# Performance work log

Hardware: AMD Instinct MI355X
Metric: run time of the kernel (lower is better)

The kernel has to match this reference:

```python
import jax, jax.numpy as jnp
import numpy as np

B, S, E = 4, 1024, 1024
H = 16
HD = E // H  # 64
NEXP = 8
FF = 4 * E
EPS = 1e-5


def _ln(x, g, b):
    m = jnp.mean(x, axis=-1, keepdims=True)
    v = jnp.var(x, axis=-1, keepdims=True)
    return (x - m) * jax.lax.rsqrt(v + EPS) * g + b


def setup_inputs() -> dict:
    key = jax.random.key(0)
    ks = jax.random.split(key, 16)
    sd = 0.02
    inp = {
        "x": jax.random.normal(ks[0], (B, S, E), jnp.float32),
        # per-head Q/K/V linears, stacked over heads: [H, E, HD]
        "wq": jax.random.normal(ks[1], (H, E, HD), jnp.float32) * sd,
        "bq": jnp.zeros((H, HD), jnp.float32),
        "wk": jax.random.normal(ks[2], (H, E, HD), jnp.float32) * sd,
        "bk": jnp.zeros((H, HD), jnp.float32),
        "wv": jax.random.normal(ks[3], (H, E, HD), jnp.float32) * sd,
        "bv": jnp.zeros((H, HD), jnp.float32),
        "wp": jax.random.normal(ks[4], (E, E), jnp.float32) * sd,
        "bp": jnp.zeros((E,), jnp.float32),
        "ln1_g": jnp.ones((E,), jnp.float32),
        "ln1_b": jnp.zeros((E,), jnp.float32),
        "ln2_g": jnp.ones((E,), jnp.float32),
        "ln2_b": jnp.zeros((E,), jnp.float32),
        "wr": jax.random.normal(ks[5], (E, NEXP), jnp.float32) * sd,
        "br": jnp.zeros((NEXP,), jnp.float32),
        # experts stacked: [NEXP, E, FF], [NEXP, FF, E]
        "w1": jax.random.normal(ks[6], (NEXP, E, FF), jnp.float32) * sd,
        "b1": jnp.zeros((NEXP, FF), jnp.float32),
        "w2": jax.random.normal(ks[7], (NEXP, FF, E), jnp.float32) * sd,
        "b2": jnp.zeros((NEXP, E), jnp.float32),
    }
    return inp


def _block(x, wq, bq, wk, bk, wv, bv, wp, bp, ln1_g, ln1_b, ln2_g, ln2_b,
           wr, br, w1, b1, w2, b2):
    # --- multi-head causal attention (per-head Q/K/V, concat, project) ---
    q = jnp.einsum('bse,hed->bhsd', x, wq) + bq[None, :, None, :]
    k = jnp.einsum('bse,hed->bhsd', x, wk) + bk[None, :, None, :]
    v = jnp.einsum('bse,hed->bhsd', x, wv) + bv[None, :, None, :]
    scores = jnp.einsum('bhsd,bhtd->bhst', q, k) / jnp.sqrt(jnp.float32(HD))
    causal = jnp.tril(jnp.ones((S, S), bool))
    scores = jnp.where(causal[None, None], scores, -jnp.inf)
    attn = jax.nn.softmax(scores, axis=-1)
    heads = jnp.einsum('bhst,bhtd->bhsd', attn, v)
    # concat heads (dim order matches torch.cat over head list)
    cat = heads.transpose(0, 2, 1, 3).reshape(B, S, E)
    attn_out = cat @ wp + bp
    # --- residual + LN1 ---
    h = _ln(attn_out + x, ln1_g, ln1_b)
    # --- MoE: router probs weight ALL experts densely (indices unused) ---
    probs = jax.nn.softmax(h @ wr + br, axis=-1)  # [B,S,NEXP]
    mid = jax.nn.relu(jnp.einsum('bse,nef->bnsf', h, w1) + b1[None, :, None, :])
    eo = jnp.einsum('bnsf,nfe->bnse', mid, w2) + b2[None, :, None, :]
    moe_out = jnp.einsum('bnse,bsn->bse', eo, probs)
    # --- residual uses ORIGINAL inputs (as in source) + LN2 ---
    return _ln(moe_out + x, ln2_g, ln2_b)


def reference(x, wq, bq, wk, bk, wv, bv, wp, bp, ln1_g, ln1_b, ln2_g, ln2_b,
              wr, br, w1, b1, w2, b2):
    return _block(x, wq, bq, wk, bk, wv, bv, wp, bp, ln1_g, ln1_b,
                  ln2_g, ln2_b, wr, br, w1, b1, w2, b2)
```

## Files before the change

kernel.cpp:

```cpp
#include <hip/hip_runtime.h>
#include <hip/hip_bf16.h>

typedef unsigned short u16;
typedef unsigned int u32;
typedef __attribute__((ext_vector_type(8))) short bf16x8;
typedef __attribute__((ext_vector_type(4))) float f32x4;

#define DEV static __device__ __forceinline__

DEV u16 f2b(float f) {
  union { float f; u32 u; } v; v.f = f;
  return (u16)((v.u + 0x7fffu + ((v.u >> 16) & 1u)) >> 16);
}

DEV void gload16(const void* g, void* l) {
  __builtin_amdgcn_global_load_lds(
      (const __attribute__((address_space(1))) u32*)g,
      (__attribute__((address_space(3))) u32*)l, 16, 0, 0);
}

__global__ __launch_bounds__(256) void cvt_bf16(const float* __restrict__ s,
                                                u16* __restrict__ d) {
  const long i = ((long)blockIdx.x * 256 + threadIdx.x) * 4;
  const float4 v = *(const float4*)&s[i];
  ushort4 o;
  o.x = f2b(v.x); o.y = f2b(v.y); o.z = f2b(v.z); o.w = f2b(v.w);
  *(ushort4*)&d[i] = o;
}

__global__ __launch_bounds__(256) void tpose_bf16(const float* __restrict__ src,
                                                  u16* __restrict__ dst, int R,
                                                  int C, long sStride,
                                                  long dStride, long ldd) {
  __shared__ float tl[32][33];
  const float* s = src + (long)blockIdx.z * sStride;
  u16* d = dst + (long)blockIdx.z * dStride;
  const int c0 = blockIdx.x * 32, r0 = blockIdx.y * 32;
  const int tx = threadIdx.x, ty = threadIdx.y;
  const int tid = ty * 32 + tx;
#pragma unroll
  for (int k = 0; k < 4; k++)
    tl[ty + k * 8][tx] = s[(long)(r0 + ty + k * 8) * C + c0 + tx];
  __syncthreads();
  const int oc = tid >> 3, orb = (tid & 7) * 4;
  ushort4 o;
  o.x = f2b(tl[orb + 0][oc]);
  o.y = f2b(tl[orb + 1][oc]);
  o.z = f2b(tl[orb + 2][oc]);
  o.w = f2b(tl[orb + 3][oc]);
  *(ushort4*)&d[(long)(c0 + oc) * ldd + r0 + orb] = o;
}

enum { EQKV, EPROJ, EFF1, EFF2, EFF2I };

template <int EPI>
__global__ __launch_bounds__(256, 3) void gemm_bt(
    const u16* __restrict__ A, const u16* __restrict__ Bt, int K, long lda,
    long ldb, const float* __restrict__ c0, const float* __restrict__ c1,
    const float* __restrict__ c2, const float* __restrict__ aux,
    float* __restrict__ fout, u16* __restrict__ o0, u16* __restrict__ o1,
    u16* __restrict__ o2, int ebase, long ldc) {
  __shared__ u16 As[12288], Bs[12288];
  long zc = 0;
  if constexpr (EPI == EFF2 || EPI == EFF2I) {
    const long z = blockIdx.z;
    A += z * (long)K;
    Bt += z * (long)K;
    fout += z * 4194304;
  }
  if constexpr (EPI == EFF1) {
    Bt += (long)blockIdx.z * 4194304;
    zc = (long)blockIdx.z * 4096;
  }
  const int tid = threadIdx.x;
  const int m0 = blockIdx.y * 128, n0 = blockIdx.x * 128;
  const int w = tid >> 6, l = tid & 63;
  const int wm = (w >> 1) * 64, wn = (w & 1) * 64;
  const int lr = l & 15, lh = l >> 4;
  f32x4 acc[4][4] = {};
  const u16* AgB = A + (long)(m0 + (tid >> 2)) * lda + (tid & 3) * 8;
  const u16* BgB = Bt + (long)(n0 + (tid >> 2)) * ldb + (tid & 3) * 8;
  const long rsA = 64 * lda, rsB = 64 * ldb;
  u16* asd = As + tid * 8;
  u16* bsd = Bs + tid * 8;
  const int nt = K >> 5;
  gload16(AgB, asd);             gload16(AgB + rsA, asd + 2048);
  gload16(BgB, bsd);             gload16(BgB + rsB, bsd + 2048);
  gload16(AgB + 32, asd + 4096); gload16(AgB + rsA + 32, asd + 6144);
  gload16(BgB + 32, bsd + 4096); gload16(BgB + rsB + 32, bsd + 6144);
  asm volatile("s_waitcnt vmcnt(4)" ::: "memory");
  __builtin_amdgcn_sched_barrier(0);
  __builtin_amdgcn_s_barrier();
  __builtin_amdgcn_sched_barrier(0);
  int oc = 0, on = 4096, ot = 8192;
  for (int t = 0; t < nt; ++t) {
    const int ks = (t + 2 < nt ? t + 2 : nt - 1) * 32;
    gload16(AgB + ks, asd + ot);
    gload16(AgB + rsA + ks, asd + ot + 2048);
    gload16(BgB + ks, bsd + ot);
    gload16(BgB + rsB + ks, bsd + ot + 2048);
    bf16x8 af[4], bfr[4];
#pragma unroll
    for (int i = 0; i < 4; i++)
      af[i] = *(const bf16x8*)&As[oc + (wm + i * 16 + lr) * 32 + lh * 8];
#pragma unroll
    for (int j = 0; j < 4; j++)
      bfr[j] = *(const bf16x8*)&Bs[oc + (wn + j * 16 + lr) * 32 + lh * 8];
    __builtin_amdgcn_s_setprio(1);
#pragma unroll
    for (int i = 0; i < 4; i++)
#pragma unroll
      for (int j = 0; j < 4; j++)
        acc[i][j] = __builtin_amdgcn_mfma_f32_16x16x32_bf16(af[i], bfr[j],
                                                            acc[i][j], 0, 0, 0);
    __builtin_amdgcn_s_setprio(0);
    asm volatile("s_waitcnt vmcnt(4)" ::: "memory");
    __builtin_amdgcn_sched_barrier(0);
    __builtin_amdgcn_s_barrier();
    __builtin_amdgcn_sched_barrier(0);
    const int tmp = oc; oc = on; on = ot; ot = tmp;
  }
  asm volatile("s_waitcnt vmcnt(0)" ::: "memory");
#pragma unroll
  for (int j = 0; j < 4; j++) {
    const int col = n0 + wn + j * 16 + lr;
#pragma unroll
    for (int i = 0; i < 4; i++)
#pragma unroll
      for (int r = 0; r < 4; r++) {
        const int row = m0 + wm + i * 16 + lh * 4 + r;
        float v = acc[i][j][r];
        if constexpr (EPI == EQKV) {
          const int which = col >> 10, hd = col & 1023;
          const float vb =
              v + ((which == 0) ? c0 : (which == 1) ? c1 : c2)[hd];
          const int b = row >> 10, s = row & 1023;
          const int h = hd >> 6, d = hd & 63;
          const long bh = b * 16 + h;
          if (which == 0)
            o0[(bh * 1024 + s) * 64 + d] = f2b(vb * 0.125f);
          else if (which == 1)
            o1[(bh * 1024 + s) * 64 + d] = f2b(vb);
          else
            o2[bh * 65536 + (long)d * 1024 + s] = f2b(vb);
        } else if constexpr (EPI == EPROJ) {
          const long idx = (long)row * 1024 + col;
          fout[idx] = v + c0[col] + aux[idx];
        } else if constexpr (EPI == EFF1) {
          const int e = ebase + blockIdx.z;
          const float t = v + c0[(long)e * 4096 + col];
          const float rl = t > 0.f ? t : 0.f;
          const float pw = aux[(long)row * 8 + e];
          o0[(long)row * ldc + zc + col] = f2b(rl * pw);
        } else {
          const long idx = (long)row * 1024 + col;
          if constexpr (EPI == EFF2I)
            fout[idx] = v;
          else
            fout[idx] = fout[idx] + v;
        }
      }
  }
}

__global__ __launch_bounds__(256) void attn_fwd(const u16* __restrict__ Qb,
                                                const u16* __restrict__ Kb,
                                                const u16* __restrict__ Vt,
                                                u16* __restrict__ Cat) {
  const int tid = threadIdx.x;
  const int w = tid >> 6, l = tid & 63;
  const int lr = l & 15, lh = l >> 4;
  const int bh = blockIdx.y;
  const int q0 = blockIdx.x * 64 + w * 16;
  const u16* Qp = Qb + (long)bh * 65536;
  const u16* Kp = Kb + (long)bh * 65536;
  const u16* Vp = Vt + (long)bh * 65536;
  const bf16x8 qf0 = *(const bf16x8*)&Qp[(q0 + lr) * 64 + lh * 8];
  const bf16x8 qf1 = *(const bf16x8*)&Qp[(q0 + lr) * 64 + 32 + lh * 8];
  const int q = q0 + lr;
  f32x4 o[4] = {};
  float m = -1e30f, ssum = 0.f;
  const int hi = lh >> 1;
  const int s0 = ((lh & 1) * 2) * 16 + lr;
  const int s1 = ((lh & 1) * 2 + 1) * 16 + lr;
  const int nkt = q0 / 32 + 1;
  for (int kt = 0; kt < nkt; kt++) {
    const int t0 = kt * 32;
    f32x4 sc[2];
#pragma unroll
    for (int ts = 0; ts < 2; ts++) {
      const bf16x8 kf0 = *(const bf16x8*)&Kp[(t0 + ts * 16 + lr) * 64 + lh * 8];
      const bf16x8 kf1 =
          *(const bf16x8*)&Kp[(t0 + ts * 16 + lr) * 64 + 32 + lh * 8];
      f32x4 c = {};
      c = __builtin_amdgcn_mfma_f32_16x16x32_bf16(kf0, qf0, c, 0, 0, 0);
      c = __builtin_amdgcn_mfma_f32_16x16x32_bf16(kf1, qf1, c, 0, 0, 0);
      sc[ts] = c;
    }
#pragma unroll
    for (int ts = 0; ts < 2; ts++)
#pragma unroll
      for (int r = 0; r < 4; r++)
        if (t0 + ts * 16 + lh * 4 + r > q) sc[ts][r] = -1e30f;
    float mt = fmaxf(fmaxf(fmaxf(sc[0][0], sc[0][1]), fmaxf(sc[0][2], sc[0][3])),
                     fmaxf(fmaxf(sc[1][0], sc[1][1]), fmaxf(sc[1][2], sc[1][3])));
    mt = fmaxf(mt, __shfl_xor(mt, 16));
    mt = fmaxf(mt, __shfl_xor(mt, 32));
    const float mnew = fmaxf(m, mt);
    const float scl = __expf(m - mnew);
    m = mnew;
    float p0[4], p1[4], ps = 0.f;
#pragma unroll
    for (int r = 0; r < 4; r++) {
      p0[r] = __expf(sc[0][r] - mnew);
      p1[r] = __expf(sc[1][r] - mnew);
      ps += p0[r] + p1[r];
    }
    ssum = ssum * scl + ps;
    u16 pb[8];
#pragma unroll
    for (int r = 0; r < 4; r++) {
      const float a0 = __shfl(p0[r], s0), b0 = __shfl(p1[r], s0);
      const float a1 = __shfl(p0[r], s1), b1 = __shfl(p1[r], s1);
      pb[r] = f2b(hi ? b0 : a0);
      pb[r + 4] = f2b(hi ? b1 : a1);
    }
#pragma unroll
    for (int dt = 0; dt < 4; dt++)
#pragma unroll
      for (int r = 0; r < 4; r++) o[dt][r] *= scl;
    const bf16x8 pf = *(const bf16x8*)pb;
    __builtin_amdgcn_s_setprio(1);
#pragma unroll
    for (int dt = 0; dt < 4; dt++) {
      const bf16x8 vf =
          *(const bf16x8*)&Vp[(dt * 16 + lr) * 1024 + t0 + lh * 8];
      o[dt] = __builtin_amdgcn_mfma_f32_16x16x32_bf16(vf, pf, o[dt], 0, 0, 0);
    }
    __builtin_amdgcn_s_setprio(0);
  }
  ssum += __shfl_xor(ssum, 16);
  ssum += __shfl_xor(ssum, 32);
  const float inv = 1.f / ssum;
  const int b = bh >> 4, h = bh & 15;
#pragma unroll
  for (int dt = 0; dt < 4; dt++) {
    ushort4 st;
    st.x = f2b(o[dt][0] * inv);
    st.y = f2b(o[dt][1] * inv);
    st.z = f2b(o[dt][2] * inv);
    st.w = f2b(o[dt][3] * inv);
    *(ushort4*)&Cat[((long)(b * 1024 + q)) * 1024 + h * 64 + dt * 16 + lh * 4] =
        st;
  }
}

DEV float wred(float v) {
#pragma unroll
  for (int d = 1; d < 64; d <<= 1) v += __shfl_xor(v, d);
  return v;
}

__global__ __launch_bounds__(256) void ln1_router(
    const float* __restrict__ in, const float* __restrict__ g,
    const float* __restrict__ bb, const float* __restrict__ wr,
    const float* __restrict__ br, u16* __restrict__ h,
    float* __restrict__ probs) {
  __shared__ float rs[4], rs2[4], rp[4][8];
  const int row = blockIdx.x, t = threadIdx.x;
  const int w = t >> 6, l = t & 63;
  const float4 v = *(const float4*)&in[(long)row * 1024 + t * 4];
  float s = v.x + v.y + v.z + v.w;
  float s2 = v.x * v.x + v.y * v.y + v.z * v.z + v.w * v.w;
  s = wred(s);
  s2 = wred(s2);
  if (l == 0) { rs[w] = s; rs2[w] = s2; }
  __syncthreads();
  const float S = rs[0] + rs[1] + rs[2] + rs[3];
  const float S2 = rs2[0] + rs2[1] + rs2[2] + rs2[3];
  const float mean = S * (1.f / 1024.f);
  const float var = S2 * (1.f / 1024.f) - mean * mean;
  const float rr = rsqrtf(var + 1e-5f);
  const float4 gv = *(const float4*)&g[t * 4];
  const float4 bv = *(const float4*)&bb[t * 4];
  float hv[4];
  hv[0] = (v.x - mean) * rr * gv.x + bv.x;
  hv[1] = (v.y - mean) * rr * gv.y + bv.y;
  hv[2] = (v.z - mean) * rr * gv.z + bv.z;
  hv[3] = (v.w - mean) * rr * gv.w + bv.w;
  ushort4 hb;
  hb.x = f2b(hv[0]); hb.y = f2b(hv[1]); hb.z = f2b(hv[2]); hb.w = f2b(hv[3]);
  *(ushort4*)&h[(long)row * 1024 + t * 4] = hb;
  float pr[8] = {};
  const float* wrp = wr + t * 4 * 8;
#pragma unroll
  for (int e = 0; e < 4; e++)
#pragma unroll
    for (int j = 0; j < 8; j++) pr[j] += hv[e] * wrp[e * 8 + j];
#pragma unroll
  for (int j = 0; j < 8; j++) pr[j] = wred(pr[j]);
  if (l == 0)
#pragma unroll
    for (int j = 0; j < 8; j++) rp[w][j] = pr[j];
  __syncthreads();
  if (t == 0) {
    float lg[8], mx = -1e30f;
#pragma unroll
    for (int j = 0; j < 8; j++) {
      lg[j] = rp[0][j] + rp[1][j] + rp[2][j] + rp[3][j] + br[j];
      mx = fmaxf(mx, lg[j]);
    }
    float sm = 0.f;
#pragma unroll
    for (int j = 0; j < 8; j++) {
      lg[j] = __expf(lg[j] - mx);
      sm += lg[j];
    }
    const float inv = 1.f / sm;
#pragma unroll
    for (int j = 0; j < 8; j++) probs[row * 8 + j] = lg[j] * inv;
  }
}

__global__ __launch_bounds__(256) void ln2_kernel(
    const float* __restrict__ moe, const float* __restrict__ xres,
    const float* __restrict__ probs, const float* __restrict__ b2,
    const float* __restrict__ g, const float* __restrict__ bb,
    float* __restrict__ out, int np) {
  __shared__ float rs[4], rs2[4];
  const int row = blockIdx.x, t = threadIdx.x;
  const int w = t >> 6, l = t & 63;
  const long base = (long)row * 1024 + t * 4;
  float4 v = *(const float4*)&xres[base];
  for (int z = 0; z < np; z++) {
    const float4 a = *(const float4*)&moe[(long)z * 4194304 + base];
    v.x += a.x; v.y += a.y; v.z += a.z; v.w += a.w;
  }
#pragma unroll
  for (int n = 0; n < 8; n++) {
    const float pw = probs[(long)row * 8 + n];
    const float4 bv4 = *(const float4*)&b2[n * 1024 + t * 4];
    v.x += pw * bv4.x; v.y += pw * bv4.y;
    v.z += pw * bv4.z; v.w += pw * bv4.w;
  }
  float s = v.x + v.y + v.z + v.w;
  float s2 = v.x * v.x + v.y * v.y + v.z * v.z + v.w * v.w;
  s = wred(s);
  s2 = wred(s2);
  if (l == 0) { rs[w] = s; rs2[w] = s2; }
  __syncthreads();
  const float S = rs[0] + rs[1] + rs[2] + rs[3];
  const float S2 = rs2[0] + rs2[1] + rs2[2] + rs2[3];
  const float mean = S * (1.f / 1024.f);
  const float var = S2 * (1.f / 1024.f) - mean * mean;
  const float rr = rsqrtf(var + 1e-5f);
  const float4 gv = *(const float4*)&g[t * 4];
  const float4 bv = *(const float4*)&bb[t * 4];
  float4 oo;
  oo.x = (v.x - mean) * rr * gv.x + bv.x;
  oo.y = (v.y - mean) * rr * gv.y + bv.y;
  oo.z = (v.z - mean) * rr * gv.z + bv.z;
  oo.w = (v.w - mean) * rr * gv.w + bv.w;
  *(float4*)&out[base] = oo;
}

extern "C" void kernel_launch(void* const* d_in, const int* in_sizes, int n_in,
                              void* d_out, int out_size, void* d_ws,
                              size_t ws_size, hipStream_t stream) {
  const float* x = (const float*)d_in[0];
  const float* wq = (const float*)d_in[1];
  const float* bq = (const float*)d_in[2];
  const float* wk = (const float*)d_in[3];
  const float* bk = (const float*)d_in[4];
  const float* wv = (const float*)d_in[5];
  const float* bv = (const float*)d_in[6];
  const float* wp = (const float*)d_in[7];
  const float* bp = (const float*)d_in[8];
  const float* g1 = (const float*)d_in[9];
  const float* be1 = (const float*)d_in[10];
  const float* g2 = (const float*)d_in[11];
  const float* be2 = (const float*)d_in[12];
  const float* wr = (const float*)d_in[13];
  const float* br = (const float*)d_in[14];
  const float* w1 = (const float*)d_in[15];
  const float* b1 = (const float*)d_in[16];
  const float* w2 = (const float*)d_in[17];
  const float* b2 = (const float*)d_in[18];
  float* out = (float*)d_out;

  char* p = (char*)d_ws;
  auto alloc = [&](size_t bytes) {
    char* r = p;
    p += (bytes + 255) & ~(size_t)255;
    return r;
  };
  u16* w1t = (u16*)alloc(67108864);
  u16* w2t2 = (u16*)alloc(67108864);
  u16* hb = (u16*)alloc(8388608);
  float* probs = (float*)alloc(131072);
  float* moe = (float*)alloc(33554432);
  float* resid1 = (float*)alloc(16777216);
  u16* xb = (u16*)alloc(8388608);
  u16* wqkvt = (u16*)alloc(6291456);
  u16* wpt = (u16*)alloc(2097152);
  u16* qb = (u16*)alloc(8388608);
  u16* kb = (u16*)alloc(8388608);
  u16* vt = (u16*)alloc(8388608);
  u16* cat = (u16*)alloc(8388608);
  const size_t need_fast = (size_t)((char*)qb - (char*)d_ws) + (size_t)268435456;
  const bool fast = ws_size >= need_fast;

  const dim3 tb(32, 8);
  cvt_bf16<<<4096, 256, 0, stream>>>(x, xb);
  tpose_bf16<<<dim3(2, 32, 16), tb, 0, stream>>>(wq, wqkvt, 1024, 64, 65536, 65536, 1024);
  tpose_bf16<<<dim3(2, 32, 16), tb, 0, stream>>>(wk, wqkvt + 1048576, 1024, 64, 65536, 65536, 1024);
  tpose_bf16<<<dim3(2, 32, 16), tb, 0, stream>>>(wv, wqkvt + 2097152, 1024, 64, 65536, 65536, 1024);
  tpose_bf16<<<dim3(32, 32, 1), tb, 0, stream>>>(wp, wpt, 1024, 1024, 0, 0, 1024);
  tpose_bf16<<<dim3(128, 32, 8), tb, 0, stream>>>(w1, w1t, 1024, 4096, 4194304, 4194304, 1024);
  tpose_bf16<<<dim3(32, 128, 8), tb, 0, stream>>>(w2, w2t2, 4096, 1024, 4194304, 4096, 32768);

  gemm_bt<EQKV><<<dim3(24, 32), 256, 0, stream>>>(
      xb, wqkvt, 1024, 1024, 1024, bq, bk, bv, nullptr, nullptr, qb, kb, vt,
      0, 0);
  attn_fwd<<<dim3(16, 64), 256, 0, stream>>>(qb, kb, vt, cat);
  gemm_bt<EPROJ><<<dim3(8, 32), 256, 0, stream>>>(
      cat, wpt, 1024, 1024, 1024, bp, nullptr, nullptr, x, resid1, nullptr,
      nullptr, nullptr, 0, 0);
  ln1_router<<<4096, 256, 0, stream>>>(resid1, g1, be1, wr, br, hb, probs);

  if (fast) {
    u16* mid = qb;
    gemm_bt<EFF1><<<dim3(32, 32, 8), 256, 0, stream>>>(
        hb, w1t, 1024, 1024, 1024, b1, nullptr, nullptr, probs, nullptr, mid,
        nullptr, nullptr, 0, 32768);
    gemm_bt<EFF2I><<<dim3(8, 32, 4), 256, 0, stream>>>(
        mid, w2t2, 8192, 32768, 32768, nullptr, nullptr, nullptr, nullptr,
        moe, nullptr, nullptr, nullptr, 0, 0);
    ln2_kernel<<<4096, 256, 0, stream>>>(moe, x, probs, b2, g2, be2, out, 4);
  } else {
    u16* mid = qb;
    for (int n = 0; n < 8; n++) {
      gemm_bt<EFF1><<<dim3(32, 32, 1), 256, 0, stream>>>(
          hb, w1t + (long)n * 4194304, 1024, 1024, 1024, b1, nullptr, nullptr,
          probs, nullptr, mid, nullptr, nullptr, n, 4096);
      if (n == 0)
        gemm_bt<EFF2I><<<dim3(8, 32, 2), 256, 0, stream>>>(
            mid, w2t2 + (long)n * 4096, 2048, 4096, 32768, nullptr, nullptr,
            nullptr, nullptr, moe, nullptr, nullptr, nullptr, 0, 0);
      else
        gemm_bt<EFF2><<<dim3(8, 32, 2), 256, 0, stream>>>(
            mid, w2t2 + (long)n * 4096, 2048, 4096, 32768, nullptr, nullptr,
            nullptr, nullptr, moe, nullptr, nullptr, nullptr, 0, 0);
    }
    ln2_kernel<<<4096, 256, 0, stream>>>(moe, x, probs, b2, g2, be2, out, 2);
  }
}
```

Baseline: 1.502 ms.

## Switch GEMM to double-buffered LDS with swizzle, block remap, and higher occupancy

Replaces the triple-buffered LDS pipeline with a double buffer, cutting shared memory per block so the launch bound can request four blocks per CU instead of three. It adds an XOR swizzle on the LDS column index to reduce bank conflicts on fragment reads. It also remaps block indices so consecutive blocks spread across tile groups, aiming for better L2 reuse. The s_setprio hints and explicit vmcnt waits are dropped in favour of __syncthreads, which shortens prefetch distance and may expose more load latency.

```diff
diff --git a/kernel.cpp b/kernel.cpp
--- a/kernel.cpp
+++ b/kernel.cpp
@@ -54,13 +54,13 @@
 enum { EQKV, EPROJ, EFF1, EFF2, EFF2I };
 
 template <int EPI>
-__global__ __launch_bounds__(256, 3) void gemm_bt(
+__global__ __launch_bounds__(256, 4) void gemm_bt(
     const u16* __restrict__ A, const u16* __restrict__ Bt, int K, long lda,
     long ldb, const float* __restrict__ c0, const float* __restrict__ c1,
     const float* __restrict__ c2, const float* __restrict__ aux,
     float* __restrict__ fout, u16* __restrict__ o0, u16* __restrict__ o1,
     u16* __restrict__ o2, int ebase, long ldc) {
-  __shared__ u16 As[12288], Bs[12288];
+  __shared__ u16 As[8192], Bs[8192];
   long zc = 0;
   if constexpr (EPI == EFF2 || EPI == EFF2I) {
     const long z = blockIdx.z;
@@ -72,55 +72,53 @@
     Bt += (long)blockIdx.z * 4194304;
     zc = (long)blockIdx.z * 4096;
   }
+  const int gx = gridDim.x, cpx = (gx * gridDim.y) >> 3;
+  const int lin = blockIdx.x + gx * blockIdx.y;
+  const int swz = (lin & 7) * cpx + (lin >> 3);
+  const int m0 = (swz / gx) * 128, n0 = (swz % gx) * 128;
   const int tid = threadIdx.x;
-  const int m0 = blockIdx.y * 128, n0 = blockIdx.x * 128;
   const int w = tid >> 6, l = tid & 63;
   const int wm = (w >> 1) * 64, wn = (w & 1) * 64;
   const int lr = l & 15, lh = l >> 4;
   f32x4 acc[4][4] = {};
-  const u16* AgB = A + (long)(m0 + (tid >> 2)) * lda + (tid & 3) * 8;
-  const u16* BgB = Bt + (long)(n0 + (tid >> 2)) * ldb + (tid & 3) * 8;
+  const int scol = ((tid & 3) * 8) ^ (((tid >> 2) & 3) << 3);
+  const u16* Ag = A + (long)(m0 + (tid >> 2)) * lda + scol;
+  const u16* Bg = Bt + (long)(n0 + (tid >> 2)) * ldb + scol;
   const long rsA = 64 * lda, rsB = 64 * ldb;
   u16* asd = As + tid * 8;
   u16* bsd = Bs + tid * 8;
   const int nt = K >> 5;
-  gload16(AgB, asd);             gload16(AgB + rsA, asd + 2048);
-  gload16(BgB, bsd);             gload16(BgB + rsB, bsd + 2048);
-  gload16(AgB + 32, asd + 4096); gload16(AgB + rsA + 32, asd + 6144);
-  gload16(BgB + 32, bsd + 4096); gload16(BgB + rsB + 32, bsd + 6144);
-  asm volatile("s_waitcnt vmcnt(4)" ::: "memory");
-  __builtin_amdgcn_sched_barrier(0);
-  __builtin_amdgcn_s_barrier();
-  __builtin_amdgcn_sched_barrier(0);
-  int oc = 0, on = 4096, ot = 8192;
+  gload16(Ag, asd);  gload16(Ag + rsA, asd + 2048);
+  gload16(Bg, bsd);  gload16(Bg + rsB, bsd + 2048);
+  __syncthreads();
+  int cur = 0;
+  const int cswz = (lh * 8) ^ ((lr & 3) << 3);
   for (int t = 0; t < nt; ++t) {
-    const int ks = (t + 2 < nt ? t + 2 : nt - 1) * 32;
-    gload16(AgB + ks, asd + ot);
-    gload16(AgB + rsA + ks, asd + ot + 2048);
-    gload16(BgB + ks, bsd + ot);
-    gload16(BgB + rsB + ks, bsd + ot + 2048);
+    if (t + 1 < nt) {
+      const int ks = (t + 1) * 32;
+      const int od = (cur ^ 1) * 4096;
+      gload16(Ag + ks, asd + od);
+      gload16(Ag + rsA + ks, asd + od + 2048);
+      gload16(Bg + ks, bsd + od);
+      gload16(Bg + rsB + ks, bsd + od + 2048);
+    }
+    const int ob = cur * 4096;
     bf16x8 af[4], bfr[4];
 #pragma unroll
     for (int i = 0; i < 4; i++)
-      af[i] = *(const bf16x8*)&As[oc + (wm + i * 16 + lr) * 32 + lh * 8];
+      af[i] = *(const bf16x8*)&As[ob + (wm + i * 16 + lr) * 32 + cswz];
 #pragma unroll
     for (int j = 0; j < 4; j++)
-      bfr[j] = *(const bf16x8*)&Bs[oc + (wn + j * 16 + lr) * 32 + lh * 8];
-    __builtin_amdgcn_s_setprio(1);
+      bfr[j] = *(const bf16x8*)&Bs[ob + (wn + j * 16 + lr) * 32 + cswz];
 #pragma unroll
     for (int i = 0; i < 4; i++)
 #pragma unroll
       for (int j = 0; j < 4; j++)
         acc[i][j] = __builtin_amdgcn_mfma_f32_16x16x32_bf16(af[i], bfr[j],
                                                             acc[i][j], 0, 0, 0);
-    __builtin_amdgcn_s_setprio(0);
-    asm volatile("s_waitcnt vmcnt(4)" ::: "memory");
-    __builtin_amdgcn_sched_barrier(0);
-    __builtin_amdgcn_s_barrier();
-    __builtin_amdgcn_sched_barrier(0);
-    const int tmp = oc; oc = on; on = ot; ot = tmp;
-  }
-  asm volatile("s_waitcnt vmcnt(0)" ::: "memory");
+    __syncthreads();
+    cur ^= 1;
+  }
 #pragma unroll
   for (int j = 0; j < 4; j++) {
     const int col = n0 + wn + j * 16 + lr;
```

New measurement: 1.394 ms. 7.2% less time.
